# Kernel optimization log

Hardware: AMD Instinct MI355X
Metric: run time of the kernel (lower is better)

Reference implementation:

```python
import jax, jax.numpy as jnp
import numpy as np

B, K, D_MODEL = 64, 256, 512
D_STATE, D_CONV, EXPAND = 16, 4, 1
D_INNER = EXPAND * D_MODEL
DT_RANK = (D_MODEL + 15) // 16  # 32
EPS = 1e-5


def _layer_norm(x, g, b):
    m = jnp.mean(x, axis=-1, keepdims=True)
    v = jnp.mean(jnp.square(x - m), axis=-1, keepdims=True)
    return (x - m) * jax.lax.rsqrt(v + EPS) * g + b


def _silu(x):
    return x * jax.nn.sigmoid(x)


def _mamba_block(x, in_proj_w, conv_w, conv_b, x_proj_w, dt_proj_w, dt_proj_b, A_log, Dp, out_proj_w):
    # x: (B, K, d_model)
    b, k, _ = x.shape
    d_inner = A_log.shape[0]
    d_state = A_log.shape[1]
    dt_rank = dt_proj_w.shape[1]
    xz = x @ in_proj_w.T                      # (B, K, 2*d_inner)
    xi, z = jnp.split(xz, 2, axis=-1)
    # causal depthwise conv1d, width d_conv
    pad = conv_w.shape[1] - 1
    xp = jnp.pad(xi, ((0, 0), (pad, 0), (0, 0)))
    xc = conv_b + sum(xp[:, w:w + k, :] * conv_w[:, w] for w in range(conv_w.shape[1]))
    xc = _silu(xc)
    proj = xc @ x_proj_w.T                    # (B, K, dt_rank + 2*d_state)
    dtr = proj[..., :dt_rank]
    Bc = proj[..., dt_rank:dt_rank + d_state]  # (B, K, d_state)
    Cc = proj[..., dt_rank + d_state:]         # (B, K, d_state)
    dt = jax.nn.softplus(dtr @ dt_proj_w.T + dt_proj_b)  # (B, K, d_inner)
    A = -jnp.exp(A_log)                       # (d_inner, d_state)

    def step(h, inp):
        dt_t, x_t, B_t, C_t = inp             # (B,d_inner),(B,d_inner),(B,d_state),(B,d_state)
        dA = jnp.exp(dt_t[:, :, None] * A)    # (B, d_inner, d_state)
        h = dA * h + (dt_t * x_t)[:, :, None] * B_t[:, None, :]
        y = jnp.einsum('bds,bs->bd', h, C_t)
        return h, y

    h0 = jnp.zeros((b, d_inner, d_state), x.dtype)
    xs = (dt.transpose(1, 0, 2), xc.transpose(1, 0, 2),
          Bc.transpose(1, 0, 2), Cc.transpose(1, 0, 2))
    _, ys = jax.lax.scan(step, h0, xs)        # ys: (K, B, d_inner)
    y = ys.transpose(1, 0, 2) + xc * Dp       # skip term D*x
    y = y * _silu(z)
    return y @ out_proj_w.T


def setup_inputs() -> dict:
    key = jax.random.key(0)
    ks = jax.random.split(key, 8)
    s = 0.02
    slots = jax.random.normal(ks[0], (B, K, D_MODEL), dtype=jnp.float32)
    in_proj_w = jax.random.normal(ks[1], (2 * D_INNER, D_MODEL), jnp.float32) * s
    conv_w = jax.random.normal(ks[2], (D_INNER, D_CONV), jnp.float32) * 0.1
    conv_b = jnp.zeros((D_INNER,), jnp.float32)
    x_proj_w = jax.random.normal(ks[3], (DT_RANK + 2 * D_STATE, D_INNER), jnp.float32) * s
    dt_proj_w = jax.random.normal(ks[4], (D_INNER, DT_RANK), jnp.float32) * s
    dt_proj_b = jax.random.normal(ks[5], (D_INNER,), jnp.float32) * 0.1 - 4.0  # small softplus(dt)
    A_log = jnp.log(jnp.broadcast_to(jnp.arange(1, D_STATE + 1, dtype=jnp.float32), (D_INNER, D_STATE)))
    Dp = jnp.ones((D_INNER,), jnp.float32)
    out_proj_w = jax.random.normal(ks[6], (D_MODEL, D_INNER), jnp.float32) * s
    ln_g = jnp.ones((D_MODEL,), jnp.float32)
    ln_b = jnp.zeros((D_MODEL,), jnp.float32)
    fln_g = jnp.ones((D_MODEL,), jnp.float32)
    fln_b = jnp.zeros((D_MODEL,), jnp.float32)
    return {"slots": slots, "ln_g": ln_g, "ln_b": ln_b,
            "in_proj_w": in_proj_w, "conv_w": conv_w, "conv_b": conv_b,
            "x_proj_w": x_proj_w, "dt_proj_w": dt_proj_w, "dt_proj_b": dt_proj_b,
            "A_log": A_log, "Dp": Dp, "out_proj_w": out_proj_w,
            "fln_g": fln_g, "fln_b": fln_b}


def reference(slots, ln_g, ln_b, in_proj_w, conv_w, conv_b, x_proj_w,
              dt_proj_w, dt_proj_b, A_log, Dp, out_proj_w, fln_g, fln_b):
    x = slots
    # num_layers = 1: pre-norm -> mamba -> residual
    residual = x
    x = _layer_norm(x, ln_g, ln_b)
    x = _mamba_block(x, in_proj_w, conv_w, conv_b, x_proj_w,
                     dt_proj_w, dt_proj_b, A_log, Dp, out_proj_w)
    x = x + residual
    return _layer_norm(x, fln_g, fln_b)
```

## Files before the change

kernel.cpp:

```cpp
#include <hip/hip_runtime.h>
#include <hip/hip_bf16.h>


#define NTOK 16384
#define DM   512

typedef __attribute__((ext_vector_type(8))) short bf16x8;
typedef __attribute__((ext_vector_type(4))) float f32x4;

__device__ __forceinline__ unsigned short f2bf(float f){
  unsigned int u = __float_as_uint(f);
  u = (u + 0x7fffu + ((u >> 16) & 1u)) >> 16;
  return (unsigned short)u;
}
__device__ __forceinline__ float bfu(unsigned short p){ return __uint_as_float(((unsigned int)p) << 16); }
__device__ __forceinline__ unsigned int pk2(float a, float b){
  return (unsigned int)f2bf(a) | ((unsigned int)f2bf(b) << 16);
}
__device__ __forceinline__ float silu(float a){ return a / (1.f + __expf(-a)); }

__device__ __forceinline__ void async_cp16(const unsigned short* g, unsigned short* l){
  __builtin_amdgcn_global_load_lds(
      (const __attribute__((address_space(1))) unsigned int*)g,
      (__attribute__((address_space(3))) unsigned int*)l, 16, 0, 0);
}

__global__ __launch_bounds__(256) void k_cvtw(const float* __restrict__ W,
                                              unsigned short* __restrict__ Wb){
  int i = (blockIdx.x*256 + threadIdx.x)*8;
  float4 a = *(const float4*)(W+i);
  float4 b = *(const float4*)(W+i+4);
  uint4 st = { pk2(a.x,a.y), pk2(a.z,a.w), pk2(b.x,b.y), pk2(b.z,b.w) };
  *(uint4*)(Wb+i) = st;
}

__global__ __launch_bounds__(64) void k_ln(const float* __restrict__ x,
                                           const float* __restrict__ g,
                                           const float* __restrict__ b,
                                           unsigned short* __restrict__ out){
  int tok  = blockIdx.x;
  int lane = threadIdx.x;
  const float* row = x + (size_t)tok*DM + lane*8;
  float4 r0 = *(const float4*)row;
  float4 r1 = *(const float4*)(row + 4);
  float v[8] = {r0.x,r0.y,r0.z,r0.w, r1.x,r1.y,r1.z,r1.w};
  float s = 0.f;
  #pragma unroll
  for (int i=0;i<8;i++) s += v[i];
  #pragma unroll
  for (int o=32;o;o>>=1) s += __shfl_xor(s, o, 64);
  float m = s * (1.0f/512.0f);
  float vs = 0.f;
  #pragma unroll
  for (int i=0;i<8;i++){ float d = v[i]-m; vs += d*d; }
  #pragma unroll
  for (int o=32;o;o>>=1) vs += __shfl_xor(vs, o, 64);
  float rs = rsqrtf(vs*(1.0f/512.0f) + 1e-5f);
  float4 g0 = *(const float4*)(g + lane*8);
  float4 g1 = *(const float4*)(g + lane*8 + 4);
  float4 b0 = *(const float4*)(b + lane*8);
  float4 b1 = *(const float4*)(b + lane*8 + 4);
  float gv[8] = {g0.x,g0.y,g0.z,g0.w, g1.x,g1.y,g1.z,g1.w};
  float bv[8] = {b0.x,b0.y,b0.z,b0.w, b1.x,b1.y,b1.z,b1.w};
  float o8[8];
  #pragma unroll
  for (int i=0;i<8;i++) o8[i] = (v[i]-m)*rs*gv[i] + bv[i];
  uint4 st = { pk2(o8[0],o8[1]), pk2(o8[2],o8[3]), pk2(o8[4],o8[5]), pk2(o8[6],o8[7]) };
  *(uint4*)(out + (size_t)tok*DM + lane*8) = st;
}

__global__ __launch_bounds__(256) void k_gemm(const unsigned short* __restrict__ A,
                                              const unsigned short* __restrict__ Wb,
                                              float* __restrict__ out_f,
                                              unsigned short* __restrict__ out_b,
                                              int mode){
  __shared__ unsigned short As[2][128*32];
  __shared__ unsigned short Bs[2][128*32];
  int t0  = blockIdx.x * 128;
  int n0  = blockIdx.y * 128;
  int tid = threadIdx.x;
  int lane = tid & 63;
  int wv  = tid >> 6;
  int mw  = wv & 1, nw = wv >> 1;
  int m15 = lane & 15, quad = lane >> 4;

  int srow   = wv*32 + (lane >> 2);
  int schunk = ((lane & 3) ^ ((lane >> 3) & 3)) * 8;
  const unsigned short* gA = A  + (size_t)(t0 + srow)*DM + schunk;
  const unsigned short* gB = Wb + (size_t)(n0 + srow)*DM + schunk;
  unsigned short* asb0 = &As[0][(wv*32)*32];
  unsigned short* bsb0 = &Bs[0][(wv*32)*32];
  unsigned short* asb1 = &As[1][(wv*32)*32];
  unsigned short* bsb1 = &Bs[1][(wv*32)*32];

  async_cp16(gA,         asb0);
  async_cp16(gA + 16*DM, asb0 + 16*32);
  async_cp16(gB,         bsb0);
  async_cp16(gB + 16*DM, bsb0 + 16*32);

  f32x4 acc[4][4];
  #pragma unroll
  for (int rb=0;rb<4;rb++)
    #pragma unroll
    for (int cb=0;cb<4;cb++) acc[rb][cb] = (f32x4){0.f,0.f,0.f,0.f};

  int rdsw = (quad ^ ((m15 >> 1) & 3)) * 8;
  int cur = 0;
  for (int ks = 0; ks < 16; ks++){
    __syncthreads();
    if (ks < 15){
      const unsigned short* nA = gA + (ks+1)*32;
      const unsigned short* nB = gB + (ks+1)*32;
      unsigned short* na = cur ? asb0 : asb1;
      unsigned short* nb = cur ? bsb0 : bsb1;
      async_cp16(nA,         na);
      async_cp16(nA + 16*DM, na + 16*32);
      async_cp16(nB,         nb);
      async_cp16(nB + 16*DM, nb + 16*32);
    }
    bf16x8 af[4], bfr[4];
    #pragma unroll
    for (int rb=0;rb<4;rb++)
      af[rb] = *(const bf16x8*)&As[cur][(mw*64 + rb*16 + m15)*32 + rdsw];
    #pragma unroll
    for (int cb=0;cb<4;cb++)
      bfr[cb] = *(const bf16x8*)&Bs[cur][(nw*64 + cb*16 + m15)*32 + rdsw];
    #pragma unroll
    for (int rb=0;rb<4;rb++)
      #pragma unroll
      for (int cb=0;cb<4;cb++)
        acc[rb][cb] = __builtin_amdgcn_mfma_f32_16x16x32_bf16(af[rb], bfr[cb], acc[rb][cb], 0, 0, 0);
    cur ^= 1;
  }

  #pragma unroll
  for (int rb=0;rb<4;rb++){
    int tok0 = t0 + mw*64 + rb*16 + quad*4;
    int b    = tok0 >> 8;
    int tl0  = tok0 & 255;
    #pragma unroll
    for (int cb=0;cb<4;cb++){
      int nn = n0 + nw*64 + cb*16 + m15;
      f32x4 v = acc[rb][cb];
      if (mode == 0){
        if (nn < DM){
          *(f32x4*)(out_f + ((size_t)(b*DM + nn))*256 + tl0) = v;
        } else {
          uint2 z2 = { pk2(silu(v[0]), silu(v[1])), pk2(silu(v[2]), silu(v[3])) };
          *(uint2*)(out_b + ((size_t)(b*DM + (nn - DM)))*256 + tl0) = z2;
        }
      } else {
        #pragma unroll
        for (int r=0;r<4;r++) out_f[(size_t)(tok0+r)*DM + nn] = v[r];
      }
    }
  }
}

__global__ __launch_bounds__(256) void k_xproj(const float* __restrict__ xiT,
                                               const float* __restrict__ cw,
                                               const float* __restrict__ cb,
                                               const unsigned short* __restrict__ xpwb,
                                               const unsigned short* __restrict__ dtwb,
                                               const float* __restrict__ dtb,
                                               float* __restrict__ dtT,
                                               float* __restrict__ Bc,
                                               float* __restrict__ Cc){
  __shared__ unsigned short xcb[32*520];
  __shared__ unsigned short Bst[2][64*32];
  __shared__ unsigned short pjA[32*40];
  int t0  = blockIdx.x * 32;
  int b   = t0 >> 8;
  int tl0 = t0 & 255;
  int tid = threadIdx.x;
  int lane = tid & 63;
  int wv  = tid >> 6;
  int m15 = lane & 15, quad = lane >> 4;

  #pragma unroll
  for (int j=0;j<2;j++){
    int d = tid + 256*j;
    float4 cr = *(const float4*)(cw + d*4);
    float a0 = cb[d];
    const float* row = xiT + ((size_t)(b*DM + d))*256;
    float w[36];
    if (tl0 == 0){
      w[0]=w[1]=w[2]=w[3]=0.f;
      #pragma unroll
      for (int q2=0;q2<8;q2++){
        float4 v4 = *(const float4*)(row + q2*4);
        w[4+q2*4]=v4.x; w[5+q2*4]=v4.y; w[6+q2*4]=v4.z; w[7+q2*4]=v4.w;
      }
    } else {
      const float* p4 = row + tl0 - 4;
      #pragma unroll
      for (int q2=0;q2<9;q2++){
        float4 v4 = *(const float4*)(p4 + q2*4);
        w[q2*4]=v4.x; w[1+q2*4]=v4.y; w[2+q2*4]=v4.z; w[3+q2*4]=v4.w;
      }
    }
    #pragma unroll
    for (int t=0;t<32;t++){
      float a = a0 + w[t+1]*cr.x + w[t+2]*cr.y + w[t+3]*cr.z + w[t+4]*cr.w;
      xcb[t*520 + d] = f2bf(silu(a));
    }
  }

  int srow = wv*16 + (lane >> 2);
  int sch  = ((lane & 3) ^ ((lane >> 3) & 3)) * 8;
  async_cp16(xpwb + srow*DM + sch, &Bst[0][(wv*16)*32]);
  __syncthreads();

  int mt = wv & 1, ntp = wv >> 1;
  f32x4 pacc[2];
  pacc[0] = (f32x4){0.f,0.f,0.f,0.f};
  pacc[1] = (f32x4){0.f,0.f,0.f,0.f};
  int rdsw = (quad ^ ((m15 >> 1) & 3)) * 8;
  int cur = 0;
  for (int ks=0; ks<16; ks++){
    if (ks < 15)
      async_cp16(xpwb + srow*DM + (ks+1)*32 + sch, &Bst[cur^1][(wv*16)*32]);
    bf16x8 af = *(const bf16x8*)&xcb[(mt*16 + m15)*520 + ks*32 + quad*8];
    #pragma unroll
    for (int j2=0;j2<2;j2++){
      int nt = ntp*2 + j2;
      bf16x8 bfr = *(const bf16x8*)&Bst[cur][(nt*16 + m15)*32 + rdsw];
      pacc[j2] = __builtin_amdgcn_mfma_f32_16x16x32_bf16(af, bfr, pacc[j2], 0, 0, 0);
    }
    cur ^= 1;
    __syncthreads();
  }

  if (ntp == 0){
    #pragma unroll
    for (int j2=0;j2<2;j2++){
      int col = j2*16 + m15;
      #pragma unroll
      for (int r=0;r<4;r++)
        pjA[(mt*16 + quad*4 + r)*40 + col] = f2bf(pacc[j2][r]);
    }
  } else {
    #pragma unroll
    for (int j2=0;j2<2;j2++){
      int c = j2*16 + m15;
      #pragma unroll
      for (int r=0;r<4;r++){
        int tt = t0 + mt*16 + quad*4 + r;
        float v = pacc[j2][r];
        if (c < 16) Bc[(size_t)tt*16 + c] = v;
        else        Cc[(size_t)tt*16 + (c-16)] = v;
      }
    }
  }
  __syncthreads();

  bf16x8 adt = *(const bf16x8*)&pjA[(mt*16 + m15)*40 + quad*8];
  int nh = wv >> 1;
  #pragma unroll
  for (int j2=0;j2<16;j2++){
    int nn = (nh*16 + j2)*16 + m15;
    bf16x8 bfr = *(const bf16x8*)(dtwb + nn*32 + quad*8);
    f32x4 dacc = (f32x4){0.f,0.f,0.f,0.f};
    dacc = __builtin_amdgcn_mfma_f32_16x16x32_bf16(adt, bfr, dacc, 0, 0, 0);
    float bb = dtb[nn];
    f32x4 o;
    #pragma unroll
    for (int r=0;r<4;r++){
      float s = dacc[r] + bb;
      o[r] = (s > 20.f) ? s : log1pf(__expf(s));
    }
    *(f32x4*)(dtT + ((size_t)(b*DM + nn))*256 + tl0 + mt*16 + quad*4) = o;
  }
}

__global__ __launch_bounds__(256) void k_scan(const float* __restrict__ dtT,
                                              const float* __restrict__ xiT,
                                              const unsigned short* __restrict__ zsT,
                                              const float* __restrict__ Bc,
                                              const float* __restrict__ Cc,
                                              const float* __restrict__ cw,
                                              const float* __restrict__ cb,
                                              const float* __restrict__ Alog,
                                              const float* __restrict__ Dpw,
                                              unsigned short* __restrict__ ya){
  int tid = threadIdx.x;
  int sl  = tid & 3;
  int q   = blockIdx.x*64 + (tid >> 2);
  int d   = q & 511;
  int b   = q >> 9;
  float4 Alr = *(const float4*)(Alog + d*16 + sl*4);
  float A0 = -__expf(Alr.x), A1 = -__expf(Alr.y);
  float A2 = -__expf(Alr.z), A3 = -__expf(Alr.w);
  float Dv = Dpw[d];
  float4 cr = *(const float4*)(cw + d*4);
  float cbv = cb[d];
  float h0=0.f, h1=0.f, h2=0.f, h3=0.f;
  float xm1=0.f, xm2=0.f, xm3=0.f;
  const float* dtp = dtT + (size_t)q*256;
  const float* xip = xiT + (size_t)q*256;
  const unsigned short* zsp = zsT + (size_t)q*256;
  unsigned short* yap = ya + (size_t)b*256*DM + d;
  const float* Bp = Bc + (size_t)b*4096 + sl*4;
  const float* Cp = Cc + (size_t)b*4096 + sl*4;
  #pragma unroll 2
  for (int t0=0; t0<256; t0+=4){
    float4 dt4 = *(const float4*)(dtp + t0);
    float4 xi4 = *(const float4*)(xip + t0);
    uint2  zz  = *(const uint2*)(zsp + t0);
    float xts[4] = {xi4.x, xi4.y, xi4.z, xi4.w};
    float dvs[4] = {dt4.x, dt4.y, dt4.z, dt4.w};
    float zsf[4] = { bfu((unsigned short)zz.x), bfu((unsigned short)(zz.x>>16)),
                     bfu((unsigned short)zz.y), bfu((unsigned short)(zz.y>>16)) };
    #pragma unroll
    for (int r=0;r<4;r++){
      float4 Bv = *(const float4*)(Bp + (t0+r)*16);
      float4 Cv = *(const float4*)(Cp + (t0+r)*16);
      float a  = cbv + xm3*cr.x + xm2*cr.y + xm1*cr.z + xts[r]*cr.w;
      float u  = silu(a);
      float dv = dvs[r];
      float du = dv*u;
      h0 = __expf(dv*A0)*h0 + du*Bv.x;
      h1 = __expf(dv*A1)*h1 + du*Bv.y;
      h2 = __expf(dv*A2)*h2 + du*Bv.z;
      h3 = __expf(dv*A3)*h3 + du*Bv.w;
      float yy = h0*Cv.x + h1*Cv.y + h2*Cv.z + h3*Cv.w;
      yy += __shfl_xor(yy, 1);
      yy += __shfl_xor(yy, 2);
      if (sl == 0) yap[(size_t)(t0+r)*DM] = f2bf((yy + u*Dv) * zsf[r]);
      xm3 = xm2; xm2 = xm1; xm1 = xts[r];
    }
  }
}

__global__ __launch_bounds__(64) void k_fln(const float* __restrict__ o,
                                            const float* __restrict__ resid,
                                            const float* __restrict__ g,
                                            const float* __restrict__ b,
                                            float* __restrict__ out){
  int tok  = blockIdx.x;
  int lane = threadIdx.x;
  const float* row = o     + (size_t)tok*DM + lane*8;
  const float* rr  = resid + (size_t)tok*DM + lane*8;
  float4 r0 = *(const float4*)row;
  float4 r1 = *(const float4*)(row + 4);
  float4 s0 = *(const float4*)rr;
  float4 s1 = *(const float4*)(rr + 4);
  float v[8] = {r0.x+s0.x, r0.y+s0.y, r0.z+s0.z, r0.w+s0.w,
                r1.x+s1.x, r1.y+s1.y, r1.z+s1.z, r1.w+s1.w};
  float s = 0.f;
  #pragma unroll
  for (int i=0;i<8;i++) s += v[i];
  #pragma unroll
  for (int o2=32;o2;o2>>=1) s += __shfl_xor(s, o2, 64);
  float m = s * (1.0f/512.0f);
  float vs = 0.f;
  #pragma unroll
  for (int i=0;i<8;i++){ float d = v[i]-m; vs += d*d; }
  #pragma unroll
  for (int o2=32;o2;o2>>=1) vs += __shfl_xor(vs, o2, 64);
  float rs = rsqrtf(vs*(1.0f/512.0f) + 1e-5f);
  float4 g0 = *(const float4*)(g + lane*8);
  float4 g1 = *(const float4*)(g + lane*8 + 4);
  float4 b0 = *(const float4*)(b + lane*8);
  float4 b1 = *(const float4*)(b + lane*8 + 4);
  float gv[8] = {g0.x,g0.y,g0.z,g0.w, g1.x,g1.y,g1.z,g1.w};
  float bv[8] = {b0.x,b0.y,b0.z,b0.w, b1.x,b1.y,b1.z,b1.w};
  float o8[8];
  #pragma unroll
  for (int i=0;i<8;i++) o8[i] = (v[i]-m)*rs*gv[i] + bv[i];
  float4* op = (float4*)(out + (size_t)tok*DM + lane*8);
  op[0] = make_float4(o8[0],o8[1],o8[2],o8[3]);
  op[1] = make_float4(o8[4],o8[5],o8[6],o8[7]);
}

extern "C" void kernel_launch(void* const* d_in, const int* in_sizes, int n_in,
                              void* d_out, int out_size, void* d_ws, size_t ws_size,
                              hipStream_t stream) {
  const float* slots     = (const float*)d_in[0];
  const float* ln_g      = (const float*)d_in[1];
  const float* ln_b      = (const float*)d_in[2];
  const float* in_proj_w = (const float*)d_in[3];
  const float* conv_w    = (const float*)d_in[4];
  const float* conv_b    = (const float*)d_in[5];
  const float* x_proj_w  = (const float*)d_in[6];
  const float* dt_proj_w = (const float*)d_in[7];
  const float* dt_proj_b = (const float*)d_in[8];
  const float* A_log     = (const float*)d_in[9];
  const float* Dp        = (const float*)d_in[10];
  const float* out_projw = (const float*)d_in[11];
  const float* fln_g     = (const float*)d_in[12];
  const float* fln_b     = (const float*)d_in[13];
  float* out = (float*)d_out;

  const size_t MB = 1024*1024;
  char* base = (char*)d_ws;
  float*          xiT  = (float*)(base);
  unsigned short* xlnb = (unsigned short*)(base + 32*MB);
  unsigned short* yab  = xlnb;
  unsigned short* xpwb = xlnb;
  unsigned short* dtwb = xlnb + 32768;
  unsigned short* zsT  = (unsigned short*)(base + 48*MB);
  unsigned short* WbO  = zsT;
  float*          dto  = (float*)(base + 64*MB);
  unsigned short* WbI  = (unsigned short*)dto;
  float*          Bc   = (float*)(base + 96*MB);
  float*          Cc   = (float*)(base + 97*MB);

  k_ln   <<<NTOK,           64, 0, stream>>>(slots, ln_g, ln_b, xlnb);
  k_cvtw <<<256,           256, 0, stream>>>(in_proj_w, WbI);
  k_gemm <<<dim3(128, 8),  256, 0, stream>>>(xlnb, WbI, xiT, zsT, 0);
  k_cvtw <<<16,            256, 0, stream>>>(x_proj_w, xpwb);
  k_cvtw <<<8,             256, 0, stream>>>(dt_proj_w, dtwb);
  k_xproj<<<NTOK/32,       256, 0, stream>>>(xiT, conv_w, conv_b, xpwb, dtwb, dt_proj_b,
                                             dto, Bc, Cc);
  k_scan <<<512,           256, 0, stream>>>(dto, xiT, zsT, Bc, Cc, conv_w, conv_b, A_log, Dp, yab);
  k_cvtw <<<128,           256, 0, stream>>>(out_projw, WbO);
  k_gemm <<<dim3(128, 4),  256, 0, stream>>>(yab, WbO, dto, (unsigned short*)0, 1);
  k_fln  <<<NTOK,           64, 0, stream>>>(dto, slots, fln_g, fln_b, out);
}
```

Baseline: 319.4 us.

## Software-pipeline scan loads and use DPP reductions with spread output stores

Restructures the selective-scan kernel to double-buffer the per-4-step loads of dt, x, z, B and C, issuing the next group's loads before computing the current group. It also replaces the shfl_xor reductions with DPP quad reductions, folds log2(e) into A so exp2f is used, and has each of the four lanes in a quad store one of the four timestep outputs, instead of lane 0 storing all four. The aim is to hide global load latency behind the serial recurrence and to cut shuffle and store-divergence overhead. The cost is higher register pressure from the two live load buffers.

```diff
diff --git a/kernel.cpp b/kernel.cpp
--- a/kernel.cpp
+++ b/kernel.cpp
@@ -18,6 +18,12 @@
   return (unsigned int)f2bf(a) | ((unsigned int)f2bf(b) << 16);
 }
 __device__ __forceinline__ float silu(float a){ return a / (1.f + __expf(-a)); }
+
+__device__ __forceinline__ float qsum(float x){
+  x += __int_as_float(__builtin_amdgcn_mov_dpp(__float_as_int(x), 0xB1, 0xF, 0xF, true));
+  x += __int_as_float(__builtin_amdgcn_mov_dpp(__float_as_int(x), 0x4E, 0xF, 0xF, true));
+  return x;
+}
 
 __device__ __forceinline__ void async_cp16(const unsigned short* g, unsigned short* l){
   __builtin_amdgcn_global_load_lds(
@@ -273,6 +279,46 @@
   }
 }
 
+#define SCAN_STEP(DV, XT, BV, CV, ZS, OUT) do {                                 \
+    float a_ = fmaf((XT),cr.w, fmaf(xm1,cr.z, fmaf(xm2,cr.y, fmaf(xm3,cr.x, cbv)))); \
+    float u_ = a_ / (1.f + __expf(-a_));                                        \
+    float dv_ = (DV);                                                           \
+    float du_ = dv_*u_;                                                         \
+    h0 = fmaf(exp2f(dv_*A0), h0, du_*(BV).x);                                   \
+    h1 = fmaf(exp2f(dv_*A1), h1, du_*(BV).y);                                   \
+    h2 = fmaf(exp2f(dv_*A2), h2, du_*(BV).z);                                   \
+    h3 = fmaf(exp2f(dv_*A3), h3, du_*(BV).w);                                   \
+    float yy_ = fmaf(h3,(CV).w, fmaf(h2,(CV).z, fmaf(h1,(CV).y, h0*(CV).x)));   \
+    yy_ = qsum(yy_);                                                            \
+    OUT = fmaf(u_, Dv, yy_) * (ZS);                                             \
+    xm3 = xm2; xm2 = xm1; xm1 = (XT);                                           \
+  } while(0)
+
+#define SCAN_LOAD(DT4, XI4, ZZ, B0,B1,B2,B3, C0,C1,C2,C3) do {                  \
+    DT4 = *(const float4*)dtp;  XI4 = *(const float4*)xip;                      \
+    ZZ  = *(const uint2*)zsp;                                                   \
+    B0 = *(const float4*)(Bp);    B1 = *(const float4*)(Bp+16);                 \
+    B2 = *(const float4*)(Bp+32); B3 = *(const float4*)(Bp+48);                 \
+    C0 = *(const float4*)(Cp);    C1 = *(const float4*)(Cp+16);                 \
+    C2 = *(const float4*)(Cp+32); C3 = *(const float4*)(Cp+48);                 \
+    dtp += 4; xip += 4; zsp += 4; Bp += 64; Cp += 64;                           \
+  } while(0)
+
+#define SCAN_BODY(DT4, XI4, ZZ, B0,B1,B2,B3, C0,C1,C2,C3) do {                  \
+    float zs0_ = __uint_as_float((ZZ).x << 16);                                 \
+    float zs1_ = __uint_as_float((ZZ).x & 0xffff0000u);                         \
+    float zs2_ = __uint_as_float((ZZ).y << 16);                                 \
+    float zs3_ = __uint_as_float((ZZ).y & 0xffff0000u);                         \
+    float o0_,o1_,o2_,o3_;                                                      \
+    SCAN_STEP((DT4).x,(XI4).x,B0,C0,zs0_,o0_);                                  \
+    SCAN_STEP((DT4).y,(XI4).y,B1,C1,zs1_,o1_);                                  \
+    SCAN_STEP((DT4).z,(XI4).z,B2,C2,zs2_,o2_);                                  \
+    SCAN_STEP((DT4).w,(XI4).w,B3,C3,zs3_,o3_);                                  \
+    float osel_ = (sl==0)?o0_:(sl==1)?o1_:(sl==2)?o2_:o3_;                      \
+    *yo = f2bf(osel_);                                                          \
+    yo += 4*DM;                                                                 \
+  } while(0)
+
 __global__ __launch_bounds__(256) void k_scan(const float* __restrict__ dtT,
                                               const float* __restrict__ xiT,
                                               const unsigned short* __restrict__ zsT,
@@ -288,9 +334,10 @@
   int q   = blockIdx.x*64 + (tid >> 2);
   int d   = q & 511;
   int b   = q >> 9;
+  const float LOG2E = 1.44269504f;
   float4 Alr = *(const float4*)(Alog + d*16 + sl*4);
-  float A0 = -__expf(Alr.x), A1 = -__expf(Alr.y);
-  float A2 = -__expf(Alr.z), A3 = -__expf(Alr.w);
+  float A0 = -__expf(Alr.x)*LOG2E, A1 = -__expf(Alr.y)*LOG2E;
+  float A2 = -__expf(Alr.z)*LOG2E, A3 = -__expf(Alr.w)*LOG2E;
   float Dv = Dpw[d];
   float4 cr = *(const float4*)(cw + d*4);
   float cbv = cb[d];
@@ -299,36 +346,20 @@
   const float* dtp = dtT + (size_t)q*256;
   const float* xip = xiT + (size_t)q*256;
   const unsigned short* zsp = zsT + (size_t)q*256;
-  unsigned short* yap = ya + (size_t)b*256*DM + d;
+  unsigned short* yo = ya + (size_t)b*256*DM + d + sl*DM;
   const float* Bp = Bc + (size_t)b*4096 + sl*4;
   const float* Cp = Cc + (size_t)b*4096 + sl*4;
-  #pragma unroll 2
-  for (int t0=0; t0<256; t0+=4){
-    float4 dt4 = *(const float4*)(dtp + t0);
-    float4 xi4 = *(const float4*)(xip + t0);
-    uint2  zz  = *(const uint2*)(zsp + t0);
-    float xts[4] = {xi4.x, xi4.y, xi4.z, xi4.w};
-    float dvs[4] = {dt4.x, dt4.y, dt4.z, dt4.w};
-    float zsf[4] = { bfu((unsigned short)zz.x), bfu((unsigned short)(zz.x>>16)),
-                     bfu((unsigned short)zz.y), bfu((unsigned short)(zz.y>>16)) };
-    #pragma unroll
-    for (int r=0;r<4;r++){
-      float4 Bv = *(const float4*)(Bp + (t0+r)*16);
-      float4 Cv = *(const float4*)(Cp + (t0+r)*16);
-      float a  = cbv + xm3*cr.x + xm2*cr.y + xm1*cr.z + xts[r]*cr.w;
-      float u  = silu(a);
-      float dv = dvs[r];
-      float du = dv*u;
-      h0 = __expf(dv*A0)*h0 + du*Bv.x;
-      h1 = __expf(dv*A1)*h1 + du*Bv.y;
-      h2 = __expf(dv*A2)*h2 + du*Bv.z;
-      h3 = __expf(dv*A3)*h3 + du*Bv.w;
-      float yy = h0*Cv.x + h1*Cv.y + h2*Cv.z + h3*Cv.w;
-      yy += __shfl_xor(yy, 1);
-      yy += __shfl_xor(yy, 2);
-      if (sl == 0) yap[(size_t)(t0+r)*DM] = f2bf((yy + u*Dv) * zsf[r]);
-      xm3 = xm2; xm2 = xm1; xm1 = xts[r];
-    }
+
+  float4 dtA, xiA, a0,a1,a2,a3, e0,e1,e2,e3; uint2 zzA;
+  float4 dtB, xiB, f0,f1,f2,f3, g0,g1,g2,g3; uint2 zzB;
+
+  SCAN_LOAD(dtA,xiA,zzA, a0,a1,a2,a3, e0,e1,e2,e3);
+  for (int it = 0; it < 64; it += 2){
+    SCAN_LOAD(dtB,xiB,zzB, f0,f1,f2,f3, g0,g1,g2,g3);
+    SCAN_BODY(dtA,xiA,zzA, a0,a1,a2,a3, e0,e1,e2,e3);
+    if (it < 62)
+      SCAN_LOAD(dtA,xiA,zzA, a0,a1,a2,a3, e0,e1,e2,e3);
+    SCAN_BODY(dtB,xiB,zzB, f0,f1,f2,f3, g0,g1,g2,g3);
   }
 }
 
```

After: 301.6 us. -5.6%, faster.
